# Kernel optimization log

Measured on AMD Instinct MI355X. Metric: run time of the kernel, lower is better.

The kernel has to match this reference:

```python
import jax, jax.numpy as jnp
import numpy as np

N_NODES = 50000
N_EDGES = 800000
D_IN = 768
D_H = 256
N_CLASSES = 4
N_LAYERS = 3
N_GRAPHS = 64
LN_EPS = 1e-5


def setup_inputs() -> dict:
    key = jax.random.key(0)
    ks = jax.random.split(key, 12)
    x = jax.random.normal(ks[0], (N_NODES, D_IN), dtype=jnp.float32)
    edge_index = jax.random.randint(ks[1], (2, N_EDGES), 0, N_NODES)
    batch = jnp.sort(jax.random.randint(ks[2], (N_NODES,), 0, N_GRAPHS))
    s_in = 1.0 / np.sqrt(D_IN)
    s_h = 1.0 / np.sqrt(D_H)
    W_in = jax.random.normal(ks[3], (D_IN, D_H), jnp.float32) * s_in
    b_in = jnp.zeros((D_H,), jnp.float32)
    convW = jax.random.normal(ks[4], (N_LAYERS, D_H, D_H), jnp.float32) * s_h
    convB = jnp.zeros((N_LAYERS, D_H), jnp.float32)
    lnG = jnp.ones((N_LAYERS, D_H), jnp.float32)
    lnB = jnp.zeros((N_LAYERS, D_H), jnp.float32)
    clsW1 = jax.random.normal(ks[5], (D_H, D_H), jnp.float32) * s_h
    clsB1 = jnp.zeros((D_H,), jnp.float32)
    clsW2 = jax.random.normal(ks[6], (D_H, N_CLASSES), jnp.float32) * s_h
    clsB2 = jnp.zeros((N_CLASSES,), jnp.float32)
    return {"x": x, "edge_index": edge_index, "batch": batch,
            "W_in": W_in, "b_in": b_in, "convW": convW, "convB": convB,
            "lnG": lnG, "lnB": lnB, "clsW1": clsW1, "clsB1": clsB1,
            "clsW2": clsW2, "clsB2": clsB2}


def _layer_norm(h, g, b):
    mu = jnp.mean(h, axis=-1, keepdims=True)
    var = jnp.mean(jnp.square(h - mu), axis=-1, keepdims=True)
    return (h - mu) * jax.lax.rsqrt(var + LN_EPS) * g + b


def reference(x, edge_index, batch, W_in, b_in, convW, convB, lnG, lnB,
              clsW1, clsB1, clsW2, clsB2):
    N = x.shape[0]
    loops = jnp.arange(N)
    src = jnp.concatenate([edge_index[0], loops])  # self-loops (PyG GCNConv default)
    dst = jnp.concatenate([edge_index[1], loops])
    deg = jax.ops.segment_sum(jnp.ones_like(src, dtype=x.dtype), dst, num_segments=N)
    dinv = jax.lax.rsqrt(deg)  # deg >= 1 due to self-loops
    norm = dinv[src] * dinv[dst]  # symmetric GCN normalization per edge

    h = x @ W_in + b_in  # input projection -> [N, D_H]
    for i in range(N_LAYERS):
        m = h @ convW[i]  # transform then propagate
        h_new = jax.ops.segment_sum(m[src] * norm[:, None], dst, num_segments=N) + convB[i]
        h = jax.nn.relu(h_new + h)  # residual (shapes match), then ReLU
        h = _layer_norm(h, lnG[i], lnB[i])
        # dropout: identity (inference mode)

    g = jax.ops.segment_max(h, batch, num_segments=N_GRAPHS)  # global_max_pool
    z = jax.nn.relu(g @ clsW1 + clsB1)
    return z @ clsW2 + clsB2  # [N_GRAPHS, N_CLASSES]
```

## Files before the change

### kernel.cpp

```cpp
#include <hip/hip_runtime.h>
#include <hip/hip_bf16.h>
#include <math.h>

#define NNODES 50000
#define NEDGES 800000
#define DIN 768
#define DH 256
#define NCLS 4
#define NGRAPHS 64
#define SCAN_BLOCKS 196

typedef __bf16 bf16x8 __attribute__((ext_vector_type(8)));
typedef float f32x4 __attribute__((ext_vector_type(4)));

static __device__ __forceinline__ float bf2f(unsigned short u) {
    union { unsigned u32; float f; } v; v.u32 = ((unsigned)u) << 16; return v.f;
}
static __device__ __forceinline__ unsigned short f2bf(float f) {
    union { float f; unsigned u; } v; v.f = f;
    unsigned r = (v.u + 0x7fffu + ((v.u >> 16) & 1u)) >> 16;
    return (unsigned short)r;
}
static __device__ __forceinline__ void unpack8(uint4 u, float* f) {
    f[0] = bf2f((unsigned short)(u.x & 0xffff)); f[1] = bf2f((unsigned short)(u.x >> 16));
    f[2] = bf2f((unsigned short)(u.y & 0xffff)); f[3] = bf2f((unsigned short)(u.y >> 16));
    f[4] = bf2f((unsigned short)(u.z & 0xffff)); f[5] = bf2f((unsigned short)(u.z >> 16));
    f[6] = bf2f((unsigned short)(u.w & 0xffff)); f[7] = bf2f((unsigned short)(u.w >> 16));
}
static __device__ __forceinline__ void gload_lds16(const void* g, void* l) {
    __builtin_amdgcn_global_load_lds((const __attribute__((address_space(1))) void*)g,
                                     (__attribute__((address_space(3))) void*)l, 16, 0, 0);
}

__global__ void detect_dtype(const unsigned short* __restrict__ x, int* __restrict__ flag) {
    __shared__ int cnt_s;
    if (threadIdx.x == 0) cnt_s = 0;
    __syncthreads();
    int c = 0;
    for (int i = 0; i < 16; ++i) {
        float v = bf2f(x[threadIdx.x * 16 + i]);
        if (!(fabsf(v) < 1e10f)) c++;
    }
    atomicAdd(&cnt_s, c);
    __syncthreads();
    if (threadIdx.x == 0) flag[0] = (cnt_s > 32) ? 1 : 0;
}

static __device__ __forceinline__ unsigned short cload(const void* src, int i, int fp32) {
    return fp32 ? f2bf(((const float*)src)[i]) : ((const unsigned short*)src)[i];
}

__global__ void canon_small(const void* b_in, const void* convB, const void* lnG,
                            const void* lnB, const void* W1, const void* W2,
                            const void* b1, const void* b2,
                            unsigned short* __restrict__ dst, const int* __restrict__ flag) {
    int i = blockIdx.x * 256 + threadIdx.x;
    if (i >= 69380) return;
    const int fp32 = flag[0];
    int j = i;
    if (j < 256)  { dst[i] = cload(b_in, j, fp32); return; }  j -= 256;
    if (j < 768)  { dst[i] = cload(convB, j, fp32); return; } j -= 768;
    if (j < 768)  { dst[i] = cload(lnG, j, fp32); return; }   j -= 768;
    if (j < 768)  { dst[i] = cload(lnB, j, fp32); return; }   j -= 768;
    if (j < 65536){ dst[i] = cload(W1, j, fp32); return; }    j -= 65536;
    if (j < 1024) { dst[i] = cload(W2, j, fp32); return; }    j -= 1024;
    if (j < 256)  { dst[i] = cload(b1, j, fp32); return; }    j -= 256;
    dst[i] = cload(b2, j, fp32);
}

__global__ void transpose_win(const void* __restrict__ src, unsigned short* __restrict__ dst,
                              const int* __restrict__ flag) {
    int idx = blockIdx.x * 256 + threadIdx.x;
    if (idx < DIN * DH) {
        int r = idx / DH, c = idx % DH;
        dst[(size_t)c * DIN + r] = cload(src, idx, flag[0]);
    }
}
__global__ void transpose_convw(const void* __restrict__ src, unsigned short* __restrict__ dst,
                                const int* __restrict__ flag) {
    int idx = blockIdx.x * 256 + threadIdx.x;
    if (idx < 3 * DH * DH) {
        int l = idx >> 16, rc = idx & 65535;
        int r = rc >> 8, c = rc & 255;
        dst[(l << 16) + c * DH + r] = cload(src, idx, flag[0]);
    }
}

__global__ void fill_sentinel(float* out, int n) {
    int i = blockIdx.x * 256 + threadIdx.x;
    if (i < n) out[i] = 1000.0f;
}

__global__ void count_edges(const int* __restrict__ ei, int* __restrict__ cnt) {
    int e = blockIdx.x * 256 + threadIdx.x;
    if (e < NEDGES) atomicAdd(&cnt[ei[NEDGES + e]], 1);
}

__global__ void scan_local(const int* __restrict__ cnt, int* __restrict__ rowptr,
                           int* __restrict__ bsum) {
    __shared__ int tmp[256];
    int i = blockIdx.x * 256 + threadIdx.x;
    int v = (i < NNODES) ? cnt[i] : 0;
    tmp[threadIdx.x] = v;
    __syncthreads();
    for (int off = 1; off < 256; off <<= 1) {
        int a = (threadIdx.x >= off) ? tmp[threadIdx.x - off] : 0;
        __syncthreads();
        tmp[threadIdx.x] += a;
        __syncthreads();
    }
    if (i < NNODES) rowptr[i] = tmp[threadIdx.x] - v;
    if (threadIdx.x == 255) bsum[blockIdx.x] = tmp[255];
}
__global__ void scan_bsum(const int* __restrict__ bsum, int* __restrict__ boff) {
    __shared__ int tmp[256];
    int t = threadIdx.x;
    int v = (t < SCAN_BLOCKS) ? bsum[t] : 0;
    tmp[t] = v;
    __syncthreads();
    for (int off = 1; off < 256; off <<= 1) {
        int a = (t >= off) ? tmp[t - off] : 0;
        __syncthreads();
        tmp[t] += a;
        __syncthreads();
    }
    if (t < SCAN_BLOCKS) boff[t] = tmp[t] - v;
}
__global__ void scan_finish(int* __restrict__ rowptr, const int* __restrict__ boff,
                            const int* __restrict__ cnt, float* __restrict__ dinv) {
    int i = blockIdx.x * 256 + threadIdx.x;
    if (i < NNODES) {
        rowptr[i] += boff[blockIdx.x];
        dinv[i] = rsqrtf((float)(1 + cnt[i]));
    }
    if (i == 0) rowptr[NNODES] = NEDGES;
}

__global__ void fill_csr(const int* __restrict__ ei, const int* __restrict__ rowptr,
                         int* __restrict__ cursor, int* __restrict__ csrc) {
    int e = blockIdx.x * 256 + threadIdx.x;
    if (e < NEDGES) {
        int s = ei[e];
        int d = ei[NEDGES + e];
        int pos = rowptr[d] + atomicAdd(&cursor[d], 1);
        csrc[pos] = s;
    }
}

template<int WF>
__global__ __launch_bounds__(256, WF ? 3 : 4) void gemm_core(
    const void* __restrict__ Araw, const int* __restrict__ dflag,
    const unsigned short* __restrict__ Bt, const unsigned short* __restrict__ bias,
    unsigned short* __restrict__ C, int M, int K)
{
    __shared__ __align__(16) char As[2][WF ? 8192 : 4096];
    __shared__ __align__(16) char Bs[2][16384];

    const int af32 = WF ? dflag[0] : 0;
    const int m0 = blockIdx.x * 64;
    const int t = threadIdx.x, wave = t >> 6, lane = t & 63;
    const int quad = lane >> 4, l16 = lane & 15;

    const char* bsrc[4];
#pragma unroll
    for (int li = 0; li < 4; ++li) {
        int c = wave * 256 + li * 64 + lane;
        int r = c >> 2, p = c & 3;
        int l = p ^ ((r >> 1) & 3);
        bsrc[li] = (const char*)Bt + ((size_t)r * K + l * 8) * 2;
    }
    const char* asrc[2];
    if (af32) {
#pragma unroll
        for (int li = 0; li < 2; ++li) {
            int c = wave * 128 + li * 64 + lane;
            int r = c >> 3, p = c & 7;
            int l = p ^ (r & 7);
            int rg = min(m0 + r, M - 1);
            asrc[li] = (const char*)Araw + ((size_t)rg * K + l * 4) * 4;
        }
    } else {
        int c = wave * 64 + lane;
        int r = c >> 2, p = c & 3;
        int l = p ^ ((r >> 1) & 3);
        int rg = min(m0 + r, M - 1);
        asrc[0] = (const char*)Araw + ((size_t)rg * K + l * 8) * 2;
        asrc[1] = asrc[0];
    }

    f32x4 acc[4][4];
#pragma unroll
    for (int i = 0; i < 4; i++)
#pragma unroll
        for (int j = 0; j < 4; j++) acc[i][j] = (f32x4){0.f, 0.f, 0.f, 0.f};

    {
#pragma unroll
        for (int li = 0; li < 4; ++li)
            gload_lds16(bsrc[li], &Bs[0][(wave * 256 + li * 64) * 16]);
        if (af32) {
            gload_lds16(asrc[0], &As[0][(wave * 128) * 16]);
            gload_lds16(asrc[1], &As[0][(wave * 128 + 64) * 16]);
        } else {
            gload_lds16(asrc[0], &As[0][(wave * 64) * 16]);
        }
    }
    __syncthreads();

    const int nt = K / 32;
    for (int tt = 0; tt < nt; ++tt) {
        const int buf = tt & 1;
        if (tt + 1 < nt) {
            const size_t k0 = (size_t)(tt + 1) * 32;
#pragma unroll
            for (int li = 0; li < 4; ++li)
                gload_lds16(bsrc[li] + k0 * 2, &Bs[buf ^ 1][(wave * 256 + li * 64) * 16]);
            if (af32) {
                gload_lds16(asrc[0] + k0 * 4, &As[buf ^ 1][(wave * 128) * 16]);
                gload_lds16(asrc[1] + k0 * 4, &As[buf ^ 1][(wave * 128 + 64) * 16]);
            } else {
                gload_lds16(asrc[0] + k0 * 2, &As[buf ^ 1][(wave * 64) * 16]);
            }
        }
        const char* as_ = As[buf];
        const char* bs_ = Bs[buf];
        bf16x8 afv[4], bfv[4];
        if (af32) {
#pragma unroll
            for (int i = 0; i < 4; i++) {
                const int row = 16 * i + l16;
                const int ph0 = (quad * 2) ^ (row & 7);
                float4 x0 = *(const float4*)(as_ + row * 128 + ph0 * 16);
                float4 x1 = *(const float4*)(as_ + row * 128 + (ph0 ^ 1) * 16);
                union { bf16x8 v; __bf16 e[8]; } u;
                u.e[0] = (__bf16)x0.x; u.e[1] = (__bf16)x0.y;
                u.e[2] = (__bf16)x0.z; u.e[3] = (__bf16)x0.w;
                u.e[4] = (__bf16)x1.x; u.e[5] = (__bf16)x1.y;
                u.e[6] = (__bf16)x1.z; u.e[7] = (__bf16)x1.w;
                afv[i] = u.v;
            }
        } else {
            const int ph = (quad ^ ((l16 >> 1) & 3)) * 16;
#pragma unroll
            for (int i = 0; i < 4; i++)
                afv[i] = *(const bf16x8*)(as_ + (16 * i + l16) * 64 + ph);
        }
        {
            const int ph = (quad ^ ((l16 >> 1) & 3)) * 16;
#pragma unroll
            for (int j = 0; j < 4; j++)
                bfv[j] = *(const bf16x8*)(bs_ + (wave * 64 + 16 * j + l16) * 64 + ph);
        }
#pragma unroll
        for (int i = 0; i < 4; i++)
#pragma unroll
            for (int j = 0; j < 4; j++)
                acc[i][j] = __builtin_amdgcn_mfma_f32_16x16x32_bf16(afv[i], bfv[j], acc[i][j], 0, 0, 0);
        __syncthreads();
    }

#pragma unroll
    for (int j = 0; j < 4; j++) {
        const int gc = wave * 64 + 16 * j + l16;
        const float bv = bias ? bf2f(bias[gc]) : 0.f;
#pragma unroll
        for (int i = 0; i < 4; i++) {
#pragma unroll
            for (int rr = 0; rr < 4; rr++) {
                int gr = m0 + 16 * i + quad * 4 + rr;
                if (gr < M) C[(size_t)gr * 256 + gc] = f2bf(acc[i][j][rr] + bv);
            }
        }
    }
}

__global__ __launch_bounds__(256) void aggregate_ln(
    const int* __restrict__ rowptr, const int* __restrict__ csrc,
    const float* __restrict__ dinv, const unsigned short* __restrict__ m,
    const unsigned short* __restrict__ convB,
    const unsigned short* __restrict__ lnG, const unsigned short* __restrict__ lnB,
    unsigned short* __restrict__ h)
{
    const int half = threadIdx.x >> 5;
    const int lane = threadIdx.x & 31;
    const int node = blockIdx.x * 8 + half;
    const float di = dinv[node];
    const size_t base = (size_t)node * DH + lane * 8;
    const size_t lo = lane * 8;

    float v0[8], v1[8], v2[8], v3[8];
    unpack8(*(const uint4*)(m + base), v0);
    const float selfn = di * di;
#pragma unroll
    for (int j = 0; j < 8; j++) { v0[j] *= selfn; v1[j] = 0.f; v2[j] = 0.f; v3[j] = 0.f; }

    const int kb = rowptr[node], ke = rowptr[node + 1];
    int k = kb;
    for (; k + 4 <= ke; k += 4) {
        const int s0 = csrc[k], s1 = csrc[k + 1], s2 = csrc[k + 2], s3 = csrc[k + 3];
        const uint4 r0 = *(const uint4*)(m + (size_t)s0 * DH + lo);
        const uint4 r1 = *(const uint4*)(m + (size_t)s1 * DH + lo);
        const uint4 r2 = *(const uint4*)(m + (size_t)s2 * DH + lo);
        const uint4 r3 = *(const uint4*)(m + (size_t)s3 * DH + lo);
        const float n0 = dinv[s0] * di, n1 = dinv[s1] * di;
        const float n2 = dinv[s2] * di, n3 = dinv[s3] * di;
        float t0[8], t1[8], t2[8], t3[8];
        unpack8(r0, t0); unpack8(r1, t1); unpack8(r2, t2); unpack8(r3, t3);
#pragma unroll
        for (int j = 0; j < 8; j++) {
            v0[j] += t0[j] * n0;
            v1[j] += t1[j] * n1;
            v2[j] += t2[j] * n2;
            v3[j] += t3[j] * n3;
        }
    }
    for (; k < ke; ++k) {
        const int s = csrc[k];
        const uint4 r = *(const uint4*)(m + (size_t)s * DH + lo);
        const float n = dinv[s] * di;
        float tv[8];
        unpack8(r, tv);
#pragma unroll
        for (int j = 0; j < 8; j++) v0[j] += tv[j] * n;
    }
#pragma unroll
    for (int j = 0; j < 8; j++) v0[j] += (v1[j] + v2[j]) + v3[j];

    float hv[8], cv[8];
    unpack8(*(const uint4*)(h + base), hv);
    unpack8(*(const uint4*)(convB + lo), cv);
    float s1 = 0.f, s2 = 0.f;
#pragma unroll
    for (int j = 0; j < 8; j++) {
        v0[j] = fmaxf(v0[j] + cv[j] + hv[j], 0.f);
        s1 += v0[j];
        s2 += v0[j] * v0[j];
    }
#pragma unroll
    for (int off = 16; off > 0; off >>= 1) {
        s1 += __shfl_xor(s1, off, 32);
        s2 += __shfl_xor(s2, off, 32);
    }
    const float mu = s1 * (1.f / 256.f);
    const float var = s2 * (1.f / 256.f) - mu * mu;
    const float rs = rsqrtf(var + 1e-5f);
    float gv[8], bv[8];
    unpack8(*(const uint4*)(lnG + lo), gv);
    unpack8(*(const uint4*)(lnB + lo), bv);
    unsigned short o[8];
#pragma unroll
    for (int j = 0; j < 8; j++) o[j] = f2bf((v0[j] - mu) * rs * gv[j] + bv[j]);
    uint4 outp;
    outp.x = (unsigned)o[0] | ((unsigned)o[1] << 16);
    outp.y = (unsigned)o[2] | ((unsigned)o[3] << 16);
    outp.z = (unsigned)o[4] | ((unsigned)o[5] << 16);
    outp.w = (unsigned)o[6] | ((unsigned)o[7] << 16);
    *(uint4*)(h + base) = outp;
}

__global__ void find_bounds(const int* __restrict__ batch, int* __restrict__ s) {
    int i = blockIdx.x * 256 + threadIdx.x;
    if (i >= NNODES) return;
    int b = batch[i];
    int bp = (i == 0) ? -1 : batch[i - 1];
    for (int g = bp + 1; g <= b; ++g) s[g] = i;
    if (i == NNODES - 1)
        for (int g = b + 1; g <= NGRAPHS; ++g) s[g] = NNODES;
}

#define PSPLIT 8
__global__ __launch_bounds__(256) void pool_partial(
    const unsigned short* __restrict__ h, const int* __restrict__ s,
    float* __restrict__ pg)
{
    const int b = blockIdx.x >> 3, split = blockIdx.x & 7, f = threadIdx.x;
    const int i0 = s[b], i1 = s[b + 1];
    const int len = i1 - i0;
    const int c0 = i0 + (int)(((long)len * split) >> 3);
    const int c1 = i0 + (int)(((long)len * (split + 1)) >> 3);
    float mx = -INFINITY;
    for (int i = c0; i < c1; ++i) mx = fmaxf(mx, bf2f(h[(size_t)i * DH + f]));
    pg[(size_t)blockIdx.x * DH + f] = mx;
}
__global__ __launch_bounds__(256) void pool_reduce(const float* __restrict__ pg,
                                                   float* __restrict__ g) {
    const int b = blockIdx.x, f = threadIdx.x;
    float mx = -INFINITY;
#pragma unroll
    for (int j = 0; j < PSPLIT; ++j) mx = fmaxf(mx, pg[(size_t)(b * PSPLIT + j) * DH + f]);
    g[b * DH + f] = mx;
}

__global__ __launch_bounds__(256) void classifier(
    const float* __restrict__ g, const unsigned short* __restrict__ W1,
    const unsigned short* __restrict__ b1, const unsigned short* __restrict__ W2,
    const unsigned short* __restrict__ b2, void* __restrict__ outv,
    const int* __restrict__ flag)
{
    __shared__ float gz[DH];
    __shared__ float zz[DH];
    const int b = blockIdx.x, t = threadIdx.x;
    gz[t] = g[b * DH + t];
    __syncthreads();
    float s = bf2f(b1[t]);
    for (int k = 0; k < DH; ++k) s += gz[k] * bf2f(W1[k * DH + t]);
    zz[t] = fmaxf(s, 0.f);
    __syncthreads();
    if (t < NCLS) {
        float s2 = bf2f(b2[t]);
        for (int k = 0; k < DH; ++k) s2 += zz[k] * bf2f(W2[k * NCLS + t]);
        if (flag[0]) ((float*)outv)[b * NCLS + t] = s2;
        else ((unsigned short*)outv)[b * NCLS + t] = f2bf(s2);
    }
}

extern "C" void kernel_launch(void* const* d_in, const int* in_sizes, int n_in,
                              void* d_out, int out_size, void* d_ws, size_t ws_size,
                              hipStream_t stream)
{
    const void* x      = d_in[0];
    const int* ei      = (const int*)d_in[1];
    const int* batch   = (const int*)d_in[2];
    const void* Win    = d_in[3];
    const void* b_in   = d_in[4];
    const void* convW  = d_in[5];
    const void* convB  = d_in[6];
    const void* lnG    = d_in[7];
    const void* lnB    = d_in[8];
    const void* W1     = d_in[9];
    const void* b1     = d_in[10];
    const void* W2     = d_in[11];
    const void* b2     = d_in[12];

    char* ws = (char*)d_ws;
    unsigned short* h   = (unsigned short*)(ws + 0);
    unsigned short* m   = (unsigned short*)(ws + 25600000);
    int* csrc           = (int*)(ws + 51200000);
    int* rowptr         = (int*)(ws + 54400000);
    int* cnt            = (int*)(ws + 54600016);
    int* cursor         = (int*)(ws + 54800016);
    float* dinv         = (float*)(ws + 55000016);
    unsigned short* cw  = (unsigned short*)(ws + 55200016);
    unsigned short* WinT= (unsigned short*)(ws + 55338784);
    unsigned short* WcT = (unsigned short*)(ws + 55732000);
    float* g            = (float*)(ws + 56125216);
    float* pg           = (float*)(ws + 56190752);
    int* gb             = (int*)(ws + 56715040);
    int* bsum           = (int*)(ws + 56715312);
    int* boff           = (int*)(ws + 56716112);
    int* flag           = (int*)(ws + 56716912);
    const size_t NEED   = 56716928;
    if (ws_size < NEED) {
        fill_sentinel<<<(out_size / 2 + 255) / 256, 256, 0, stream>>>((float*)d_out, out_size / 2);
        return;
    }

    unsigned short* cBin   = cw + 0;
    unsigned short* cConvB = cw + 256;
    unsigned short* cLnG   = cw + 1024;
    unsigned short* cLnB   = cw + 1792;
    unsigned short* cW1    = cw + 2560;
    unsigned short* cW2    = cw + 68096;
    unsigned short* cB1    = cw + 69120;
    unsigned short* cB2    = cw + 69376;

    detect_dtype<<<1, 256, 0, stream>>>((const unsigned short*)x, flag);

    hipMemsetAsync(cnt, 0, 400000, stream);
    count_edges<<<(NEDGES + 255) / 256, 256, 0, stream>>>(ei, cnt);
    scan_local<<<SCAN_BLOCKS, 256, 0, stream>>>(cnt, rowptr, bsum);
    scan_bsum<<<1, 256, 0, stream>>>(bsum, boff);
    scan_finish<<<SCAN_BLOCKS, 256, 0, stream>>>(rowptr, boff, cnt, dinv);
    fill_csr<<<(NEDGES + 255) / 256, 256, 0, stream>>>(ei, rowptr, cursor, csrc);

    canon_small<<<(69380 + 255) / 256, 256, 0, stream>>>(b_in, convB, lnG, lnB, W1, W2, b1, b2, cw, flag);
    transpose_win<<<(DIN * DH + 255) / 256, 256, 0, stream>>>(Win, WinT, flag);
    transpose_convw<<<(3 * DH * DH + 255) / 256, 256, 0, stream>>>(convW, WcT, flag);

    const int GBLK = (NNODES + 63) / 64;
    gemm_core<1><<<GBLK, 256, 0, stream>>>(x, flag, WinT, cBin, h, NNODES, DIN);

    for (int i = 0; i < 3; i++) {
        gemm_core<0><<<GBLK, 256, 0, stream>>>(h, flag, WcT + i * DH * DH, nullptr, m,
                                               NNODES, DH);
        aggregate_ln<<<NNODES / 8, 256, 0, stream>>>(
            rowptr, csrc, dinv, m, cConvB + i * DH, cLnG + i * DH, cLnB + i * DH, h);
    }

    find_bounds<<<(NNODES + 255) / 256, 256, 0, stream>>>(batch, gb);
    pool_partial<<<NGRAPHS * PSPLIT, 256, 0, stream>>>(h, gb, pg);
    pool_reduce<<<NGRAPHS, 256, 0, stream>>>(pg, g);
    classifier<<<NGRAPHS, 256, 0, stream>>>(g, cW1, cB1, cW2, cB2, d_out, flag);
}
```

Baseline: 689.0 us.

## Prescale messages by dinv in GEMM and pre-pack input into swizzled bf16 tiles

The conv GEMM epilogue now multiplies each output row by dinv[src], so aggregation becomes a plain unweighted sum scaled once by dinv[dst]. This removes the per-edge dinv gather and multiply, and the gather loop is widened to eight neighbours per iteration. Separately, the input x is converted and packed into a pre-swizzled bf16 tile layout by a new kernel, so the input GEMM streams contiguous 4KB chunks. The cost is an extra pass over x and about 77MB of extra workspace, with a fallback to the old path when the workspace is too small. Rounding also changes slightly because the scaling is applied before the bf16 store.

```diff
diff --git a/kernel.cpp b/kernel.cpp
--- a/kernel.cpp
+++ b/kernel.cpp
@@ -9,6 +9,8 @@
 #define NCLS 4
 #define NGRAPHS 64
 #define SCAN_BLOCKS 196
+#define PBLK 782
+#define PS 24
 
 typedef __bf16 bf16x8 __attribute__((ext_vector_type(8)));
 typedef float f32x4 __attribute__((ext_vector_type(4)));
@@ -26,6 +28,20 @@
     f[2] = bf2f((unsigned short)(u.y & 0xffff)); f[3] = bf2f((unsigned short)(u.y >> 16));
     f[4] = bf2f((unsigned short)(u.z & 0xffff)); f[5] = bf2f((unsigned short)(u.z >> 16));
     f[6] = bf2f((unsigned short)(u.w & 0xffff)); f[7] = bf2f((unsigned short)(u.w >> 16));
+}
+static __device__ __forceinline__ void acc8(uint4 u, float* f) {
+    f[0] += bf2f((unsigned short)(u.x & 0xffff)); f[1] += bf2f((unsigned short)(u.x >> 16));
+    f[2] += bf2f((unsigned short)(u.y & 0xffff)); f[3] += bf2f((unsigned short)(u.y >> 16));
+    f[4] += bf2f((unsigned short)(u.z & 0xffff)); f[5] += bf2f((unsigned short)(u.z >> 16));
+    f[6] += bf2f((unsigned short)(u.w & 0xffff)); f[7] += bf2f((unsigned short)(u.w >> 16));
+}
+static __device__ __forceinline__ uint4 pack8f(float4 f0, float4 f1) {
+    uint4 u;
+    u.x = (unsigned)f2bf(f0.x) | ((unsigned)f2bf(f0.y) << 16);
+    u.y = (unsigned)f2bf(f0.z) | ((unsigned)f2bf(f0.w) << 16);
+    u.z = (unsigned)f2bf(f1.x) | ((unsigned)f2bf(f1.y) << 16);
+    u.w = (unsigned)f2bf(f1.z) | ((unsigned)f2bf(f1.w) << 16);
+    return u;
 }
 static __device__ __forceinline__ void gload_lds16(const void* g, void* l) {
     __builtin_amdgcn_global_load_lds((const __attribute__((address_space(1))) void*)g,
@@ -86,6 +102,33 @@
     }
 }
 
+__global__ __launch_bounds__(256) void pack_a(
+    const void* __restrict__ x, const int* __restrict__ flag,
+    uint4* __restrict__ out)
+{
+    const int c = blockIdx.x * 256 + threadIdx.x;
+    const int blk = c / 6144;
+    const int rem = c - blk * 6144;
+    const int s = rem >> 8;
+    const int q = rem & 255;
+    const int r = q >> 2, p = q & 3;
+    const int l = p ^ ((r >> 1) & 3);
+    const int row = blk * 64 + r;
+    const int k0 = s * 32 + l * 8;
+    uint4 v = make_uint4(0u, 0u, 0u, 0u);
+    if (row < NNODES) {
+        if (flag[0]) {
+            const float* xf = (const float*)x + (size_t)row * DIN + k0;
+            float4 f0 = *(const float4*)xf;
+            float4 f1 = *(const float4*)(xf + 4);
+            v = pack8f(f0, f1);
+        } else {
+            v = *(const uint4*)((const unsigned short*)x + (size_t)row * DIN + k0);
+        }
+    }
+    out[c] = v;
+}
+
 __global__ void fill_sentinel(float* out, int n) {
     int i = blockIdx.x * 256 + threadIdx.x;
     if (i < n) out[i] = 1000.0f;
@@ -148,15 +191,15 @@
 }
 
 template<int WF>
-__global__ __launch_bounds__(256, WF ? 3 : 4) void gemm_core(
+__global__ __launch_bounds__(256, WF == 1 ? 3 : 4) void gemm_core(
     const void* __restrict__ Araw, const int* __restrict__ dflag,
     const unsigned short* __restrict__ Bt, const unsigned short* __restrict__ bias,
-    unsigned short* __restrict__ C, int M, int K)
+    const float* __restrict__ prescale, unsigned short* __restrict__ C, int M, int K)
 {
-    __shared__ __align__(16) char As[2][WF ? 8192 : 4096];
+    __shared__ __align__(16) char As[2][WF == 1 ? 8192 : 4096];
     __shared__ __align__(16) char Bs[2][16384];
 
-    const int af32 = WF ? dflag[0] : 0;
+    const int af32 = (WF == 1) ? dflag[0] : 0;
     const int m0 = blockIdx.x * 64;
     const int t = threadIdx.x, wave = t >> 6, lane = t & 63;
     const int quad = lane >> 4, l16 = lane & 15;
@@ -170,7 +213,10 @@
         bsrc[li] = (const char*)Bt + ((size_t)r * K + l * 8) * 2;
     }
     const char* asrc[2];
-    if (af32) {
+    if (WF == 2) {
+        asrc[0] = (const char*)Araw + (size_t)blockIdx.x * (PS * 4096) + t * 16;
+        asrc[1] = asrc[0];
+    } else if (WF == 1 && af32) {
 #pragma unroll
         for (int li = 0; li < 2; ++li) {
             int c = wave * 128 + li * 64 + lane;
@@ -198,7 +244,7 @@
 #pragma unroll
         for (int li = 0; li < 4; ++li)
             gload_lds16(bsrc[li], &Bs[0][(wave * 256 + li * 64) * 16]);
-        if (af32) {
+        if (WF == 1 && af32) {
             gload_lds16(asrc[0], &As[0][(wave * 128) * 16]);
             gload_lds16(asrc[1], &As[0][(wave * 128 + 64) * 16]);
         } else {
@@ -215,7 +261,9 @@
 #pragma unroll
             for (int li = 0; li < 4; ++li)
                 gload_lds16(bsrc[li] + k0 * 2, &Bs[buf ^ 1][(wave * 256 + li * 64) * 16]);
-            if (af32) {
+            if (WF == 2) {
+                gload_lds16(asrc[0] + (size_t)(tt + 1) * 4096, &As[buf ^ 1][(wave * 64) * 16]);
+            } else if (WF == 1 && af32) {
                 gload_lds16(asrc[0] + k0 * 4, &As[buf ^ 1][(wave * 128) * 16]);
                 gload_lds16(asrc[1] + k0 * 4, &As[buf ^ 1][(wave * 128 + 64) * 16]);
             } else {
@@ -225,7 +273,7 @@
         const char* as_ = As[buf];
         const char* bs_ = Bs[buf];
         bf16x8 afv[4], bfv[4];
-        if (af32) {
+        if (WF == 1 && af32) {
 #pragma unroll
             for (int i = 0; i < 4; i++) {
                 const int row = 16 * i + l16;
@@ -268,7 +316,10 @@
 #pragma unroll
             for (int rr = 0; rr < 4; rr++) {
                 int gr = m0 + 16 * i + quad * 4 + rr;
-                if (gr < M) C[(size_t)gr * 256 + gc] = f2bf(acc[i][j][rr] + bv);
+                if (gr < M) {
+                    float sc = prescale ? prescale[gr] : 1.f;
+                    C[(size_t)gr * 256 + gc] = f2bf(acc[i][j][rr] * sc + bv);
+                }
             }
         }
     }
@@ -288,43 +339,39 @@
     const size_t base = (size_t)node * DH + lane * 8;
     const size_t lo = lane * 8;
 
-    float v0[8], v1[8], v2[8], v3[8];
+    float v0[8], v1[8];
     unpack8(*(const uint4*)(m + base), v0);
-    const float selfn = di * di;
-#pragma unroll
-    for (int j = 0; j < 8; j++) { v0[j] *= selfn; v1[j] = 0.f; v2[j] = 0.f; v3[j] = 0.f; }
+#pragma unroll
+    for (int j = 0; j < 8; j++) v1[j] = 0.f;
 
     const int kb = rowptr[node], ke = rowptr[node + 1];
     int k = kb;
-    for (; k + 4 <= ke; k += 4) {
-        const int s0 = csrc[k], s1 = csrc[k + 1], s2 = csrc[k + 2], s3 = csrc[k + 3];
-        const uint4 r0 = *(const uint4*)(m + (size_t)s0 * DH + lo);
-        const uint4 r1 = *(const uint4*)(m + (size_t)s1 * DH + lo);
-        const uint4 r2 = *(const uint4*)(m + (size_t)s2 * DH + lo);
-        const uint4 r3 = *(const uint4*)(m + (size_t)s3 * DH + lo);
-        const float n0 = dinv[s0] * di, n1 = dinv[s1] * di;
-        const float n2 = dinv[s2] * di, n3 = dinv[s3] * di;
-        float t0[8], t1[8], t2[8], t3[8];
-        unpack8(r0, t0); unpack8(r1, t1); unpack8(r2, t2); unpack8(r3, t3);
-#pragma unroll
-        for (int j = 0; j < 8; j++) {
-            v0[j] += t0[j] * n0;
-            v1[j] += t1[j] * n1;
-            v2[j] += t2[j] * n2;
-            v3[j] += t3[j] * n3;
-        }
-    }
-    for (; k < ke; ++k) {
-        const int s = csrc[k];
-        const uint4 r = *(const uint4*)(m + (size_t)s * DH + lo);
-        const float n = dinv[s] * di;
-        float tv[8];
-        unpack8(r, tv);
-#pragma unroll
-        for (int j = 0; j < 8; j++) v0[j] += tv[j] * n;
-    }
-#pragma unroll
-    for (int j = 0; j < 8; j++) v0[j] += (v1[j] + v2[j]) + v3[j];
+    for (; k + 8 <= ke; k += 8) {
+        int s0 = csrc[k],     s1 = csrc[k + 1], s2 = csrc[k + 2], s3 = csrc[k + 3];
+        int s4 = csrc[k + 4], s5 = csrc[k + 5], s6 = csrc[k + 6], s7 = csrc[k + 7];
+        uint4 r0 = *(const uint4*)(m + (size_t)s0 * DH + lo);
+        uint4 r1 = *(const uint4*)(m + (size_t)s1 * DH + lo);
+        uint4 r2 = *(const uint4*)(m + (size_t)s2 * DH + lo);
+        uint4 r3 = *(const uint4*)(m + (size_t)s3 * DH + lo);
+        uint4 r4 = *(const uint4*)(m + (size_t)s4 * DH + lo);
+        uint4 r5 = *(const uint4*)(m + (size_t)s5 * DH + lo);
+        uint4 r6 = *(const uint4*)(m + (size_t)s6 * DH + lo);
+        uint4 r7 = *(const uint4*)(m + (size_t)s7 * DH + lo);
+        acc8(r0, v0); acc8(r1, v1); acc8(r2, v0); acc8(r3, v1);
+        acc8(r4, v0); acc8(r5, v1); acc8(r6, v0); acc8(r7, v1);
+    }
+    for (; k + 2 <= ke; k += 2) {
+        int s0 = csrc[k], s1 = csrc[k + 1];
+        uint4 r0 = *(const uint4*)(m + (size_t)s0 * DH + lo);
+        uint4 r1 = *(const uint4*)(m + (size_t)s1 * DH + lo);
+        acc8(r0, v0); acc8(r1, v1);
+    }
+    if (k < ke) {
+        uint4 r0 = *(const uint4*)(m + (size_t)csrc[k] * DH + lo);
+        acc8(r0, v0);
+    }
+#pragma unroll
+    for (int j = 0; j < 8; j++) v0[j] = (v0[j] + v1[j]) * di;
 
     float hv[8], cv[8];
     unpack8(*(const uint4*)(h + base), hv);
@@ -449,11 +496,14 @@
     int* bsum           = (int*)(ws + 56715312);
     int* boff           = (int*)(ws + 56716112);
     int* flag           = (int*)(ws + 56716912);
-    const size_t NEED   = 56716928;
-    if (ws_size < NEED) {
+    uint4* Apack        = (uint4*)(ws + 56716928);
+    const size_t NEED_BASE = 56716928;
+    const size_t NEED_FULL = 56716928 + (size_t)PBLK * PS * 4096;
+    if (ws_size < NEED_BASE) {
         fill_sentinel<<<(out_size / 2 + 255) / 256, 256, 0, stream>>>((float*)d_out, out_size / 2);
         return;
     }
+    const bool packed = (ws_size >= NEED_FULL);
 
     unsigned short* cBin   = cw + 0;
     unsigned short* cConvB = cw + 256;
@@ -477,11 +527,15 @@
     transpose_win<<<(DIN * DH + 255) / 256, 256, 0, stream>>>(Win, WinT, flag);
     transpose_convw<<<(3 * DH * DH + 255) / 256, 256, 0, stream>>>(convW, WcT, flag);
 
-    const int GBLK = (NNODES + 63) / 64;
-    gemm_core<1><<<GBLK, 256, 0, stream>>>(x, flag, WinT, cBin, h, NNODES, DIN);
+    if (packed) {
+        pack_a<<<PBLK * PS, 256, 0, stream>>>(x, flag, Apack);
+        gemm_core<2><<<PBLK, 256, 0, stream>>>(Apack, flag, WinT, cBin, nullptr, h, NNODES, DIN);
+    } else {
+        gemm_core<1><<<PBLK, 256, 0, stream>>>(x, flag, WinT, cBin, nullptr, h, NNODES, DIN);
+    }
 
     for (int i = 0; i < 3; i++) {
-        gemm_core<0><<<GBLK, 256, 0, stream>>>(h, flag, WcT + i * DH * DH, nullptr, m,
+        gemm_core<0><<<PBLK, 256, 0, stream>>>(h, flag, WcT + i * DH * DH, nullptr, dinv, m,
                                                NNODES, DH);
         aggregate_ln<<<NNODES / 8, 256, 0, stream>>>(
             rowptr, csrc, dinv, m, cConvB + i * DH, cLnG + i * DH, cLnB + i * DH, h);
```

After: 740.3 us. +7.4%, slower.
